# Kernel tuning notes

Measured on AMD Instinct MI355X. Metric: run time of the kernel, lower is better.

The kernel has to match this reference:

```python
import jax, jax.numpy as jnp
import numpy as np

N, F_DIM, H, K, T = 4096, 256, 256, 3, 5
START, END = 10, 3  # args.len_numerical_features, args.num_class


def setup_inputs() -> dict:
    key = jax.random.key(0)
    ks = jax.random.split(key, 8)
    s = 0.05
    x = jax.random.normal(ks[0], (N, F_DIM), dtype=jnp.float32)
    adj = jax.random.randint(ks[1], (N, N, K), 0, 2, dtype=jnp.int32)
    gnn_w = jax.random.normal(ks[2], (K, F_DIM, H), dtype=jnp.float32) * s
    gnn_b = jnp.zeros((K, H), dtype=jnp.float32)
    w_ih = jax.random.normal(ks[3], (K, 4 * H, H), dtype=jnp.float32) * s
    w_hh = jax.random.normal(ks[4], (K, 4 * H, H), dtype=jnp.float32) * s
    b_ih = jnp.zeros((K, 4 * H), dtype=jnp.float32)
    b_hh = jnp.zeros((K, 4 * H), dtype=jnp.float32)
    fc_w = jax.random.normal(ks[5], (K, F_DIM, H), dtype=jnp.float32) * s
    fc_b = jnp.zeros((K, F_DIM), dtype=jnp.float32)
    return dict(x=x, gnn_w=gnn_w, gnn_b=gnn_b, w_ih=w_ih, w_hh=w_hh,
                b_ih=b_ih, b_hh=b_hh, fc_w=fc_w, fc_b=fc_b, adj=adj)


def _gcn(x, a_bin, w, b):
    # PyG GCNConv: A_hat = A + I (self-loops added on top of existing edges,
    # weight 1), out = D^-1/2 A_hat D^-1/2 (x @ W) + b
    a = a_bin + jnp.eye(N, dtype=x.dtype)
    deg = a.sum(axis=1)
    dinv = jnp.where(deg > 0, jax.lax.rsqrt(deg), 0.0)
    a_norm = dinv[:, None] * a * dinv[None, :]
    return a_norm @ (x @ w) + b


def _lstm_last(xt, w_ih, w_hh, b_ih, b_hh):
    # batch_first LSTM over T identical inputs xt [N,H]; returns h at last step
    def step(carry, _):
        h, c = carry
        g = xt @ w_ih.T + b_ih + h @ w_hh.T + b_hh
        i, f, gg, o = jnp.split(g, 4, axis=-1)  # torch gate order: i, f, g, o
        c = jax.nn.sigmoid(f) * c + jax.nn.sigmoid(i) * jnp.tanh(gg)
        h = jax.nn.sigmoid(o) * jnp.tanh(c)
        return (h, c), None
    zero = jnp.zeros((xt.shape[0], H), dtype=xt.dtype)
    (h, c), _ = jax.lax.scan(step, (zero, zero), None, length=T)
    return h


def _sig_slice(z):
    return z.at[:, START:F_DIM - END].set(jax.nn.sigmoid(z[:, START:F_DIM - END]))


def reference(x, gnn_w, gnn_b, w_ih, w_hh, b_ih, b_hh, fc_w, fc_b, adj):
    deltas, zbars = [], []
    for k in range(K):
        a_bin = (adj[:, :, k] != 0).astype(x.dtype)
        # GCN output is identical across timesteps -> compute once
        gnn_out = _gcn(x, a_bin, gnn_w[k], gnn_b[k])
        h_last = _lstm_last(gnn_out, w_ih[k], w_hh[k], b_ih[k], b_hh[k])
        delta = jnp.tanh(h_last @ fc_w[k].T + fc_b[k])  # [N, F]
        deltas.append(delta)
        zbars.append(_sig_slice(x + delta))
    delta_z = jnp.stack(deltas, -1).mean(-1)
    res_z_bar = jnp.stack(zbars, -1)  # [N, F, K]
    pred_matrix = _sig_slice(x + delta_z)
    return pred_matrix, res_z_bar, adj
```

## Files before the change

### kernel.cpp

```cpp
#include <hip/hip_runtime.h>
#include <stdint.h>

#define NN_ 4096
#define FD 256
#define HD 256
#define KC 3
#define GD 1024
#define SA 40

typedef __attribute__((ext_vector_type(4))) unsigned int vu4;
typedef __attribute__((ext_vector_type(4))) int vi4;
typedef __attribute__((ext_vector_type(4))) float vf4;
typedef __attribute__((ext_vector_type(4))) unsigned short vus4;
typedef __attribute__((ext_vector_type(8))) short short8;
typedef __attribute__((ext_vector_type(4))) float f32x4;

typedef __attribute__((address_space(1))) const void GV;
typedef __attribute__((address_space(3))) void LV;
__device__ __forceinline__ void gl16(const void* g, void* l) {
    __builtin_amdgcn_global_load_lds((GV*)g, (LV*)l, 16, 0, 0);
}

__device__ __forceinline__ float b2f(unsigned short u) {
    unsigned int v = ((unsigned int)u) << 16; float f; __builtin_memcpy(&f, &v, 4); return f;
}
__device__ __forceinline__ unsigned short f2b(float x) {
    unsigned int u; __builtin_memcpy(&u, &x, 4);
    u = (u + 0x7FFFu + ((u >> 16) & 1u)) >> 16;
    return (unsigned short)u;
}
__device__ __forceinline__ void cvt8(const float* __restrict__ g, unsigned short* o) {
    vf4 a = *(const vf4*)g, b = *(const vf4*)(g + 4);
    o[0] = f2b(a[0]); o[1] = f2b(a[1]); o[2] = f2b(a[2]); o[3] = f2b(a[3]);
    o[4] = f2b(b[0]); o[5] = f2b(b[1]); o[6] = f2b(b[2]); o[7] = f2b(b[3]);
}
__device__ __forceinline__ float sigm(float v) { return 1.f / (1.f + __expf(-v)); }

__global__ __launch_bounds__(256) void adj_pass(const int* __restrict__ adj,
        float* __restrict__ adj_out, unsigned short* __restrict__ abk,
        float* __restrict__ dinv) {
    const int i = blockIdx.x, t = threadIdx.x;
    const int* src = adj + (size_t)i * 12288;
    float* dstf = adj_out + (size_t)i * 12288;
    float s0 = 0.f, s1 = 0.f, s2 = 0.f;
#pragma unroll
    for (int it = 0; it < 4; ++it) {
        int jq = (it * 256 + t) * 4;
        vi4 a = *(const vi4*)(src + jq * 3);
        vi4 b = *(const vi4*)(src + jq * 3 + 4);
        vi4 c = *(const vi4*)(src + jq * 3 + 8);
        int vv[12] = {a[0],a[1],a[2],a[3],b[0],b[1],b[2],b[3],c[0],c[1],c[2],c[3]};
        float ff[12];
#pragma unroll
        for (int e = 0; e < 12; ++e) ff[e] = vv[e] ? 1.f : 0.f;
        vf4 w0 = {ff[0],ff[1],ff[2],ff[3]}, w1 = {ff[4],ff[5],ff[6],ff[7]}, w2 = {ff[8],ff[9],ff[10],ff[11]};
        *(vf4*)(dstf + jq * 3) = w0; *(vf4*)(dstf + jq * 3 + 4) = w1; *(vf4*)(dstf + jq * 3 + 8) = w2;
#pragma unroll
        for (int k = 0; k < 3; ++k) {
            vus4 w;
            w[0] = vv[k]     ? (unsigned short)0x3F80 : (unsigned short)0;
            w[1] = vv[3 + k] ? (unsigned short)0x3F80 : (unsigned short)0;
            w[2] = vv[6 + k] ? (unsigned short)0x3F80 : (unsigned short)0;
            w[3] = vv[9 + k] ? (unsigned short)0x3F80 : (unsigned short)0;
            *(vus4*)(abk + ((size_t)(k * NN_ + i)) * NN_ + jq) = w;
        }
        s0 += ff[0] + ff[3] + ff[6] + ff[9];
        s1 += ff[1] + ff[4] + ff[7] + ff[10];
        s2 += ff[2] + ff[5] + ff[8] + ff[11];
    }
    __shared__ float r0[256], r1[256], r2[256];
    r0[t] = s0; r1[t] = s1; r2[t] = s2;
    __syncthreads();
    for (int off = 128; off > 0; off >>= 1) {
        if (t < off) { r0[t] += r0[t + off]; r1[t] += r1[t + off]; r2[t] += r2[t + off]; }
        __syncthreads();
    }
    if (t == 0) {
        dinv[i]            = 1.f / sqrtf(1.f + r0[0]);
        dinv[NN_ + i]      = 1.f / sqrtf(1.f + r1[0]);
        dinv[2 * NN_ + i]  = 1.f / sqrtf(1.f + r2[0]);
    }
}

__global__ __launch_bounds__(256) void wcvt(const float* __restrict__ wih,
        const float* __restrict__ whh, const float* __restrict__ fcw,
        unsigned short* __restrict__ wb) {
    size_t e = ((size_t)blockIdx.x * 256 + threadIdx.x) * 8;
    const float* src; size_t off;
    if (e < 786432)       { src = wih; off = e; }
    else if (e < 1572864) { src = whh; off = e - 786432; }
    else                  { src = fcw; off = e - 1572864; }
    alignas(16) unsigned short o[8];
    cvt8(src + off, o);
    *(vu4*)(wb + e) = *(vu4*)o;
}

__global__ __launch_bounds__(256) void gemm_xw(const float* __restrict__ x,
        const float* __restrict__ gw, const float* __restrict__ dinv,
        unsigned short* __restrict__ yT) {
    __shared__ __align__(16) unsigned short sA[64 * SA], sB[64 * SA];
    const int bi = blockIdx.x, bj = blockIdx.y, k = blockIdx.z;
    const int t = threadIdx.x, lane = t & 63, wave = t >> 6;
    const int m = lane & 15, q = lane >> 4, ko = q * 8;
    const int h0 = bj * 64;
    f32x4 acc[4] = {};
    const float* A0 = x + (size_t)(bi * 64) * FD;
    const float* B0 = gw + (size_t)k * FD * HD;
    const int r = t >> 2, c8 = (t & 3) << 3;
    const int fB = t >> 3, c8B = (t & 7) << 3;
    for (int k0 = 0; k0 < FD; k0 += 32) {
        alignas(16) unsigned short tA[8], tB[8];
        cvt8(A0 + (size_t)r * FD + k0 + c8, tA);
        *(vu4*)(sA + r * SA + c8) = *(vu4*)tA;
        cvt8(B0 + (size_t)(k0 + fB) * HD + h0 + c8B, tB);
#pragma unroll
        for (int e = 0; e < 8; ++e) sB[(c8B + e) * SA + fB] = tB[e];
        __syncthreads();
        short8 af = *(const short8*)(sA + (wave * 16 + m) * SA + ko);
#pragma unroll
        for (int ct = 0; ct < 4; ++ct) {
            short8 bf = *(const short8*)(sB + (ct * 16 + m) * SA + ko);
            acc[ct] = __builtin_amdgcn_mfma_f32_16x16x32_bf16(af, bf, acc[ct], 0, 0, 0);
        }
        __syncthreads();
    }
    unsigned short* yTk = yT + (size_t)k * HD * NN_;
#pragma unroll
    for (int ct = 0; ct < 4; ++ct)
#pragma unroll
        for (int r2 = 0; r2 < 4; ++r2) {
            int col = h0 + ct * 16 + m;
            int row = bi * 64 + wave * 16 + q * 4 + r2;
            yTk[(size_t)col * NN_ + row] = f2b(acc[ct][r2] * dinv[(size_t)k * NN_ + row]);
        }
}

__global__ __launch_bounds__(256) void gemm_agg(const unsigned short* __restrict__ abk,
        const unsigned short* __restrict__ yT, unsigned short* __restrict__ pbuf) {
    __shared__ __align__(16) unsigned short sA[128 * 32], sB[128 * 32];
    const int d = blockIdx.x;
    const int w = (d & 7) * 96 + (d >> 3);
    const int bh = w & 1, bi = (w >> 1) & 31, z = w >> 6;
    const int k = z >> 2, s = z & 3;
    const int t = threadIdx.x, lane = t & 63, wave = t >> 6;
    const int wi = wave & 1, wh = wave >> 1;
    const int m = lane & 15, q = lane >> 4, ko = q * 8;
    const int i0 = bi * 128, h0 = bh * 128, jbase = s * 1024;
    f32x4 acc[4][4] = {};
    const int lrow = lane >> 2, lcol = (lane & 3) << 3;
    const unsigned short* Ag0 = abk + ((size_t)(k * NN_ + i0 + wave * 32 + lrow)) * NN_ + jbase + lcol;
    const unsigned short* Ag1 = Ag0 + (size_t)16 * NN_;
    const unsigned short* Bg0 = yT + ((size_t)(k * 256 + h0 + wave * 32 + lrow)) * NN_ + jbase + lcol;
    const unsigned short* Bg1 = Bg0 + (size_t)16 * NN_;
    unsigned short* lA0 = sA + (wave * 32) * 32;
    unsigned short* lA1 = lA0 + 16 * 32;
    unsigned short* lB0 = sB + (wave * 32) * 32;
    unsigned short* lB1 = lB0 + 16 * 32;
    for (int j0 = 0; j0 < 1024; j0 += 32) {
        gl16(Ag0 + j0, lA0);
        gl16(Ag1 + j0, lA1);
        gl16(Bg0 + j0, lB0);
        gl16(Bg1 + j0, lB1);
        __syncthreads();
        short8 af[4], bf[4];
#pragma unroll
        for (int rt = 0; rt < 4; ++rt)
            af[rt] = *(const short8*)(sA + (wi * 64 + rt * 16 + m) * 32 + ko);
#pragma unroll
        for (int ct = 0; ct < 4; ++ct)
            bf[ct] = *(const short8*)(sB + (wh * 64 + ct * 16 + m) * 32 + ko);
#pragma unroll
        for (int ct = 0; ct < 4; ++ct)
#pragma unroll
            for (int rt = 0; rt < 4; ++rt)
                acc[rt][ct] = __builtin_amdgcn_mfma_f32_16x16x32_bf16(af[rt], bf[ct], acc[rt][ct], 0, 0, 0);
        __syncthreads();
    }
    const int addself = ((bi >> 3) == s);
#pragma unroll
    for (int rt = 0; rt < 4; ++rt)
#pragma unroll
        for (int ct = 0; ct < 4; ++ct)
#pragma unroll
            for (int r2 = 0; r2 < 4; ++r2) {
                int row = i0 + wi * 64 + rt * 16 + q * 4 + r2;
                int col = h0 + wh * 64 + ct * 16 + m;
                float v = acc[rt][ct][r2];
                if (addself) v += b2f(yT[((size_t)k * 256 + col) * NN_ + row]);
                pbuf[(((size_t)s * 3 + k) * NN_ + row) * 256 + col] = f2b(v);
            }
}

__global__ __launch_bounds__(256) void agg_reduce(const unsigned short* __restrict__ pbuf,
        const float* __restrict__ dinv, const float* __restrict__ gnnb,
        unsigned short* __restrict__ xt) {
    size_t e8 = ((size_t)blockIdx.x * 256 + threadIdx.x) * 8;
    int k = (int)(e8 >> 20);
    int i = (int)((e8 >> 8) & 4095);
    int h = (int)(e8 & 255);
    float di = dinv[k * NN_ + i];
    const size_t KIH = (size_t)KC * NN_ * HD;
    alignas(16) unsigned short p0[8], p1[8], p2[8], p3[8], o[8];
    *(vu4*)p0 = *(const vu4*)(pbuf + 0 * KIH + e8);
    *(vu4*)p1 = *(const vu4*)(pbuf + 1 * KIH + e8);
    *(vu4*)p2 = *(const vu4*)(pbuf + 2 * KIH + e8);
    *(vu4*)p3 = *(const vu4*)(pbuf + 3 * KIH + e8);
#pragma unroll
    for (int e = 0; e < 8; ++e) {
        float v = b2f(p0[e]) + b2f(p1[e]) + b2f(p2[e]) + b2f(p3[e]);
        o[e] = f2b(di * v + gnnb[k * HD + h + e]);
    }
    *(vu4*)(xt + e8) = *(vu4*)o;
}

__global__ __launch_bounds__(256) void lstm_mm(const unsigned short* __restrict__ A,
        const unsigned short* __restrict__ W, const float* __restrict__ b1,
        const float* __restrict__ b2, unsigned short* __restrict__ gX2,
        float* __restrict__ cbuf, unsigned short* __restrict__ hbuf, int mode) {
    __shared__ __align__(16) unsigned short sA[128 * 32];
    __shared__ __align__(16) unsigned short sB[128 * 32];
    const int d = blockIdx.x;
    const int w = (d & 7) * 96 + (d >> 3);
    const int chb = w & 7, bn = w >> 3;
    const int t = threadIdx.x, lane = t & 63, wave = t >> 6;
    const int m = lane & 15, q = lane >> 4, ko = q * 8;
    const int kk = bn >> 5;
    f32x4 acc[2][2][4] = {};
    const int lrow = lane >> 2, lcol = (lane & 3) << 3;
    const unsigned short* A0 = A + (size_t)bn * 128 * 256;
    const unsigned short* W0 = W + (size_t)kk * GD * 256 + (size_t)chb * 32 * 256;
    const unsigned short* Ag0 = A0 + (size_t)(wave * 32 + lrow) * 256 + lcol;
    const unsigned short* Ag1 = Ag0 + 16 * 256;
    const unsigned short* Bg0 = W0 + (size_t)(wave * 256 + lrow) * 256 + lcol;
    const unsigned short* Bg1 = Bg0 + 16 * 256;
    unsigned short* lA0 = sA + (wave * 32) * 32;
    unsigned short* lA1 = lA0 + 16 * 32;
    unsigned short* lB0 = sB + (wave * 32) * 32;
    unsigned short* lB1 = lB0 + 16 * 32;
    for (int k0 = 0; k0 < 256; k0 += 32) {
        gl16(Ag0 + k0, lA0);
        gl16(Ag1 + k0, lA1);
        gl16(Bg0 + k0, lB0);
        gl16(Bg1 + k0, lB1);
        __syncthreads();
        short8 af[2];
#pragma unroll
        for (int rt = 0; rt < 2; ++rt)
            af[rt] = *(const short8*)(sA + (wave * 32 + rt * 16 + m) * 32 + ko);
#pragma unroll
        for (int g = 0; g < 4; ++g)
#pragma unroll
            for (int cc = 0; cc < 2; ++cc) {
                short8 bf = *(const short8*)(sB + (g * 32 + cc * 16 + m) * 32 + ko);
#pragma unroll
                for (int rt = 0; rt < 2; ++rt)
                    acc[rt][cc][g] = __builtin_amdgcn_mfma_f32_16x16x32_bf16(af[rt], bf, acc[rt][cc][g], 0, 0, 0);
            }
        __syncthreads();
    }
#pragma unroll
    for (int rt = 0; rt < 2; ++rt)
#pragma unroll
        for (int cc = 0; cc < 2; ++cc)
#pragma unroll
            for (int r2 = 0; r2 < 4; ++r2) {
                int row = bn * 128 + wave * 32 + rt * 16 + q * 4 + r2;
                int ch = chb * 32 + cc * 16 + m;
                size_t goff = ((size_t)row * 256 + ch) * 4;
                if (mode == 0) {
                    vus4 o;
#pragma unroll
                    for (int g = 0; g < 4; ++g) {
                        float v = acc[rt][cc][g][r2]
                                + b1[kk * GD + g * 256 + ch] + b2[kk * GD + g * 256 + ch];
                        o[g] = f2b(v);
                    }
                    *(vus4*)(gX2 + goff) = o;
                } else {
                    vus4 gv = *(const vus4*)(gX2 + goff);
                    float iv = acc[rt][cc][0][r2] + b2f(gv[0]);
                    float fv = acc[rt][cc][1][r2] + b2f(gv[1]);
                    float gg = acc[rt][cc][2][r2] + b2f(gv[2]);
                    float ov = acc[rt][cc][3][r2] + b2f(gv[3]);
                    size_t coff = (size_t)row * 256 + ch;
                    float cn = sigm(fv) * cbuf[coff] + sigm(iv) * tanhf(gg);
                    cbuf[coff] = cn;
                    hbuf[coff] = f2b(sigm(ov) * tanhf(cn));
                }
            }
}

__global__ __launch_bounds__(256) void lstm_cell0(const unsigned short* __restrict__ gX2,
        float* __restrict__ cbuf, unsigned short* __restrict__ hbuf) {
    size_t e8 = ((size_t)blockIdx.x * 256 + threadIdx.x) * 8;
    size_t gb = e8 * 4;
    alignas(16) unsigned short gx[32], h8[8];
    alignas(16) float cv[8];
#pragma unroll
    for (int v = 0; v < 4; ++v)
        *(vu4*)(gx + v * 8) = *(const vu4*)(gX2 + gb + v * 8);
#pragma unroll
    for (int e = 0; e < 8; ++e) {
        float iv = b2f(gx[e * 4 + 0]), gg = b2f(gx[e * 4 + 2]), ov = b2f(gx[e * 4 + 3]);
        float cn = sigm(iv) * tanhf(gg);
        cv[e] = cn;
        h8[e] = f2b(sigm(ov) * tanhf(cn));
    }
    *(vf4*)(cbuf + e8)     = *(vf4*)cv;
    *(vf4*)(cbuf + e8 + 4) = *(vf4*)(cv + 4);
    *(vu4*)(hbuf + e8) = *(vu4*)h8;
}

__global__ __launch_bounds__(256) void gemm_nt_ep(const unsigned short* __restrict__ A,
        const unsigned short* __restrict__ W, const float* __restrict__ b1,
        unsigned short* __restrict__ outp, int COLS, int do_tanh) {
    __shared__ __align__(16) unsigned short sA[64 * 32], sB[64 * 32];
    const int bg = blockIdx.x, bn = blockIdx.y, k = blockIdx.z;
    const int t = threadIdx.x, lane = t & 63, wave = t >> 6;
    const int m = lane & 15, q = lane >> 4, ko = q * 8;
    f32x4 acc[4] = {};
    const int lrow = lane >> 2, lcol = (lane & 3) << 3;
    const unsigned short* A0 = A + ((size_t)k * NN_ + bn * 64) * HD;
    const unsigned short* W0 = W + ((size_t)k * COLS + bg * 64) * HD;
    const unsigned short* Ag = A0 + (size_t)(wave * 16 + lrow) * HD + lcol;
    const unsigned short* Bg = W0 + (size_t)(wave * 16 + lrow) * HD + lcol;
    unsigned short* lA = sA + (wave * 16) * 32;
    unsigned short* lB = sB + (wave * 16) * 32;
    for (int k0 = 0; k0 < HD; k0 += 32) {
        gl16(Ag + k0, lA);
        gl16(Bg + k0, lB);
        __syncthreads();
        short8 af = *(const short8*)(sA + (wave * 16 + m) * 32 + ko);
#pragma unroll
        for (int ct = 0; ct < 4; ++ct) {
            short8 bf = *(const short8*)(sB + (ct * 16 + m) * 32 + ko);
            acc[ct] = __builtin_amdgcn_mfma_f32_16x16x32_bf16(af, bf, acc[ct], 0, 0, 0);
        }
        __syncthreads();
    }
#pragma unroll
    for (int ct = 0; ct < 4; ++ct)
#pragma unroll
        for (int r2 = 0; r2 < 4; ++r2) {
            int col = bg * 64 + ct * 16 + m;
            int row = bn * 64 + wave * 16 + q * 4 + r2;
            float v = acc[ct][r2];
            if (b1) v += b1[(size_t)k * COLS + col];
            if (do_tanh) v = tanhf(v);
            outp[((size_t)k * NN_ + row) * COLS + col] = f2b(v);
        }
}

__global__ __launch_bounds__(256) void final_ep(const float* __restrict__ x,
        const unsigned short* __restrict__ delta, float* __restrict__ pred,
        float* __restrict__ res) {
    int idx = blockIdx.x * 256 + threadIdx.x;
    size_t base = (size_t)idx * 8;
    int f0 = (int)(base & 255);
    alignas(16) unsigned short d0[8], d1[8], d2[8];
    alignas(16) float pr[8], rs[24];
    vf4 xa = *(const vf4*)(x + base), xb = *(const vf4*)(x + base + 4);
    float xs[8] = { xa[0], xa[1], xa[2], xa[3], xb[0], xb[1], xb[2], xb[3] };
    *(vu4*)d0 = *(const vu4*)(delta + base);
    *(vu4*)d1 = *(const vu4*)(delta + (size_t)NN_ * FD + base);
    *(vu4*)d2 = *(const vu4*)(delta + 2 * (size_t)NN_ * FD + base);
#pragma unroll
    for (int e = 0; e < 8; ++e) {
        int f = f0 + e;
        bool sg = (f >= 10) && (f < 253);
        float xf = xs[e];
        float da = b2f(d0[e]), db = b2f(d1[e]), dc = b2f(d2[e]);
        float dm = (da + db + dc) * (1.f / 3.f);
        float p = xf + dm; if (sg) p = sigm(p);
        pr[e] = p;
        float z0 = xf + da; if (sg) z0 = sigm(z0);
        float z1 = xf + db; if (sg) z1 = sigm(z1);
        float z2 = xf + dc; if (sg) z2 = sigm(z2);
        rs[e * 3 + 0] = z0; rs[e * 3 + 1] = z1; rs[e * 3 + 2] = z2;
    }
    *(vf4*)(pred + base)     = *(vf4*)pr;
    *(vf4*)(pred + base + 4) = *(vf4*)(pr + 4);
    size_t rb = base * 3;
#pragma unroll
    for (int v = 0; v < 6; ++v)
        *(vf4*)(res + rb + v * 4) = *(vf4*)(rs + v * 4);
}

extern "C" void kernel_launch(void* const* d_in, const int* in_sizes, int n_in,
                              void* d_out, int out_size, void* d_ws, size_t ws_size,
                              hipStream_t stream) {
    const float* x    = (const float*)d_in[0];
    const float* gnnw = (const float*)d_in[1];
    const float* gnnb = (const float*)d_in[2];
    const float* wih  = (const float*)d_in[3];
    const float* whh  = (const float*)d_in[4];
    const float* bih  = (const float*)d_in[5];
    const float* bhh  = (const float*)d_in[6];
    const float* fcw  = (const float*)d_in[7];
    const float* fcb  = (const float*)d_in[8];
    const int*   adj  = (const int*)d_in[9];

    float* out = (float*)d_out;
    float* out_pred = out;
    float* out_res  = out + (size_t)NN_ * FD;
    float* out_adj  = out + (size_t)NN_ * FD * 4;

    char* ws = (char*)d_ws;
    float*          dinv  = (float*)ws;
    unsigned short* R1    = (unsigned short*)(ws + 49152);
    unsigned short* R2    = (unsigned short*)(ws + 6340608);
    unsigned short* wb    = (unsigned short*)(ws + 12632064);
    unsigned short* pbuf  = (unsigned short*)(ws + 16171008);
    unsigned short* gX2   = pbuf;
    unsigned short* abk   = (unsigned short*)(ws + 41336832);
    float*          cbuf  = (float*)(ws + 142000128);
    const unsigned short* wihb = wb;
    const unsigned short* whhb = wb + 786432;
    const unsigned short* fcwb = wb + 1572864;
    (void)ws_size; (void)in_sizes; (void)n_in; (void)out_size;

    wcvt<<<dim3(864), 256, 0, stream>>>(wih, whh, fcw, wb);
    adj_pass<<<dim3(4096), 256, 0, stream>>>(adj, out_adj, abk, dinv);
    gemm_xw<<<dim3(64, 4, 3), 256, 0, stream>>>(x, gnnw, dinv, R1 );
    gemm_agg<<<dim3(768), 256, 0, stream>>>(abk, R1 , pbuf);
    agg_reduce<<<dim3(1536), 256, 0, stream>>>(pbuf, dinv, gnnb, R2 );
    lstm_mm<<<dim3(768), 256, 0, stream>>>(R2 , wihb, bih, bhh, gX2, nullptr, nullptr, 0);
    lstm_cell0<<<dim3(1536), 256, 0, stream>>>(gX2, cbuf, R1 );
    for (int tstep = 1; tstep < 5; ++tstep)
        lstm_mm<<<dim3(768), 256, 0, stream>>>(R1 , whhb, nullptr, nullptr, gX2, cbuf, R1 , 1);
    gemm_nt_ep<<<dim3(4, 64, 3), 256, 0, stream>>>(R1 , fcwb, fcb, R2 , FD, 1);
    final_ep<<<dim3(512), 256, 0, stream>>>(x, R2 , out_pred, out_res);
}
```

Measured before the change: 622.3 us.

## Bit-pack adjacency for aggregation GEMM and fuse small kernels

Adjacency masks are stored as packed bits instead of a bf16 matrix, and the aggregation GEMM expands the bits into bf16 MFMA fragments from LDS. This removes a large write and re-read of the dense bf16 adjacency. Weight conversion is merged into adj_pass, the first LSTM cell update is fused into the first gate GEMM epilogue, and the FC GEMM is fused with the final sigmoid epilogue. In exchange, the inner loop does more bit-expansion ALU work, and the fused final kernel uses fewer blocks with uncoalesced stores.

```diff
diff --git a/kernel.cpp b/kernel.cpp
--- a/kernel.cpp
+++ b/kernel.cpp
@@ -7,6 +7,7 @@
 #define KC 3
 #define GD 1024
 #define SA 40
+#define BPITCH 144
 
 typedef __attribute__((ext_vector_type(4))) unsigned int vu4;
 typedef __attribute__((ext_vector_type(4))) int vi4;
@@ -37,15 +38,30 @@
 __device__ __forceinline__ float sigm(float v) { return 1.f / (1.f + __expf(-v)); }
 
 __global__ __launch_bounds__(256) void adj_pass(const int* __restrict__ adj,
-        float* __restrict__ adj_out, unsigned short* __restrict__ abk,
-        float* __restrict__ dinv) {
+        float* __restrict__ adj_out, unsigned char* __restrict__ abits,
+        float* __restrict__ dinv,
+        const float* __restrict__ wih, const float* __restrict__ whh,
+        const float* __restrict__ fcw, unsigned short* __restrict__ wb) {
     const int i = blockIdx.x, t = threadIdx.x;
+    if (i < 864) {
+        size_t e = ((size_t)i * 256 + t) * 8;
+        const float* src; size_t off;
+        if (e < 786432)       { src = wih; off = e; }
+        else if (e < 1572864) { src = whh; off = e - 786432; }
+        else                  { src = fcw; off = e - 1572864; }
+        alignas(16) unsigned short o[8];
+        cvt8(src + off, o);
+        *(vu4*)(wb + e) = *(vu4*)o;
+    }
+    __shared__ unsigned char nib[3][1024];
+    __shared__ float r0[256], r1[256], r2[256];
     const int* src = adj + (size_t)i * 12288;
     float* dstf = adj_out + (size_t)i * 12288;
     float s0 = 0.f, s1 = 0.f, s2 = 0.f;
 #pragma unroll
     for (int it = 0; it < 4; ++it) {
-        int jq = (it * 256 + t) * 4;
+        int p = it * 256 + t;
+        int jq = p * 4;
         vi4 a = *(const vi4*)(src + jq * 3);
         vi4 b = *(const vi4*)(src + jq * 3 + 4);
         vi4 c = *(const vi4*)(src + jq * 3 + 8);
@@ -57,20 +73,23 @@
         *(vf4*)(dstf + jq * 3) = w0; *(vf4*)(dstf + jq * 3 + 4) = w1; *(vf4*)(dstf + jq * 3 + 8) = w2;
 #pragma unroll
         for (int k = 0; k < 3; ++k) {
-            vus4 w;
-            w[0] = vv[k]     ? (unsigned short)0x3F80 : (unsigned short)0;
-            w[1] = vv[3 + k] ? (unsigned short)0x3F80 : (unsigned short)0;
-            w[2] = vv[6 + k] ? (unsigned short)0x3F80 : (unsigned short)0;
-            w[3] = vv[9 + k] ? (unsigned short)0x3F80 : (unsigned short)0;
-            *(vus4*)(abk + ((size_t)(k * NN_ + i)) * NN_ + jq) = w;
+            unsigned int nb = (vv[k] ? 1u : 0u) | (vv[3 + k] ? 2u : 0u)
+                            | (vv[6 + k] ? 4u : 0u) | (vv[9 + k] ? 8u : 0u);
+            nib[k][p] = (unsigned char)nb;
         }
         s0 += ff[0] + ff[3] + ff[6] + ff[9];
         s1 += ff[1] + ff[4] + ff[7] + ff[10];
         s2 += ff[2] + ff[5] + ff[8] + ff[11];
     }
-    __shared__ float r0[256], r1[256], r2[256];
     r0[t] = s0; r1[t] = s1; r2[t] = s2;
     __syncthreads();
+#pragma unroll
+    for (int k = 0; k < 3; ++k) {
+        unsigned int b0 = (unsigned int)nib[k][t * 4 + 0] | ((unsigned int)nib[k][t * 4 + 1] << 4);
+        unsigned int b1 = (unsigned int)nib[k][t * 4 + 2] | ((unsigned int)nib[k][t * 4 + 3] << 4);
+        *(unsigned short*)(abits + ((size_t)k * NN_ + i) * 512 + t * 2) =
+            (unsigned short)(b0 | (b1 << 8));
+    }
     for (int off = 128; off > 0; off >>= 1) {
         if (t < off) { r0[t] += r0[t + off]; r1[t] += r1[t + off]; r2[t] += r2[t + off]; }
         __syncthreads();
@@ -80,19 +99,6 @@
         dinv[NN_ + i]      = 1.f / sqrtf(1.f + r1[0]);
         dinv[2 * NN_ + i]  = 1.f / sqrtf(1.f + r2[0]);
     }
-}
-
-__global__ __launch_bounds__(256) void wcvt(const float* __restrict__ wih,
-        const float* __restrict__ whh, const float* __restrict__ fcw,
-        unsigned short* __restrict__ wb) {
-    size_t e = ((size_t)blockIdx.x * 256 + threadIdx.x) * 8;
-    const float* src; size_t off;
-    if (e < 786432)       { src = wih; off = e; }
-    else if (e < 1572864) { src = whh; off = e - 786432; }
-    else                  { src = fcw; off = e - 1572864; }
-    alignas(16) unsigned short o[8];
-    cvt8(src + off, o);
-    *(vu4*)(wb + e) = *(vu4*)o;
 }
 
 __global__ __launch_bounds__(256) void gemm_xw(const float* __restrict__ x,
@@ -135,9 +141,10 @@
         }
 }
 
-__global__ __launch_bounds__(256) void gemm_agg(const unsigned short* __restrict__ abk,
+__global__ __launch_bounds__(256) void gemm_agg(const unsigned char* __restrict__ abits,
         const unsigned short* __restrict__ yT, unsigned short* __restrict__ pbuf) {
-    __shared__ __align__(16) unsigned short sA[128 * 32], sB[128 * 32];
+    __shared__ __align__(16) unsigned char bitsA[128 * BPITCH];
+    __shared__ __align__(16) unsigned short sB[128 * 32];
     const int d = blockIdx.x;
     const int w = (d & 7) * 96 + (d >> 3);
     const int bh = w & 1, bi = (w >> 1) & 31, z = w >> 6;
@@ -146,26 +153,39 @@
     const int wi = wave & 1, wh = wave >> 1;
     const int m = lane & 15, q = lane >> 4, ko = q * 8;
     const int i0 = bi * 128, h0 = bh * 128, jbase = s * 1024;
+    {
+        const int row = t >> 1, half = t & 1;
+        const unsigned char* bsrc = abits + ((size_t)k * NN_ + i0 + row) * 512 + s * 128 + half * 64;
+        unsigned char* bdst = bitsA + row * BPITCH + half * 64;
+        vu4 v0 = *(const vu4*)(bsrc);
+        vu4 v1 = *(const vu4*)(bsrc + 16);
+        vu4 v2 = *(const vu4*)(bsrc + 32);
+        vu4 v3 = *(const vu4*)(bsrc + 48);
+        *(vu4*)(bdst)      = v0;
+        *(vu4*)(bdst + 16) = v1;
+        *(vu4*)(bdst + 32) = v2;
+        *(vu4*)(bdst + 48) = v3;
+    }
     f32x4 acc[4][4] = {};
     const int lrow = lane >> 2, lcol = (lane & 3) << 3;
-    const unsigned short* Ag0 = abk + ((size_t)(k * NN_ + i0 + wave * 32 + lrow)) * NN_ + jbase + lcol;
-    const unsigned short* Ag1 = Ag0 + (size_t)16 * NN_;
     const unsigned short* Bg0 = yT + ((size_t)(k * 256 + h0 + wave * 32 + lrow)) * NN_ + jbase + lcol;
     const unsigned short* Bg1 = Bg0 + (size_t)16 * NN_;
-    unsigned short* lA0 = sA + (wave * 32) * 32;
-    unsigned short* lA1 = lA0 + 16 * 32;
     unsigned short* lB0 = sB + (wave * 32) * 32;
     unsigned short* lB1 = lB0 + 16 * 32;
+    const int arow = (wi * 64 + m) * BPITCH + q;
     for (int j0 = 0; j0 < 1024; j0 += 32) {
-        gl16(Ag0 + j0, lA0);
-        gl16(Ag1 + j0, lA1);
         gl16(Bg0 + j0, lB0);
         gl16(Bg1 + j0, lB1);
         __syncthreads();
+        const int jby = j0 >> 3;
         short8 af[4], bf[4];
 #pragma unroll
-        for (int rt = 0; rt < 4; ++rt)
-            af[rt] = *(const short8*)(sA + (wi * 64 + rt * 16 + m) * 32 + ko);
+        for (int rt = 0; rt < 4; ++rt) {
+            unsigned int by = bitsA[arow + rt * 16 * BPITCH + jby];
+#pragma unroll
+            for (int e = 0; e < 8; ++e)
+                af[rt][e] = (short)(((by >> e) & 1u) ? (short)0x3F80 : (short)0);
+        }
 #pragma unroll
         for (int ct = 0; ct < 4; ++ct)
             bf[ct] = *(const short8*)(sB + (wh * 64 + ct * 16 + m) * 32 + ko);
@@ -267,22 +287,26 @@
                 int row = bn * 128 + wave * 32 + rt * 16 + q * 4 + r2;
                 int ch = chb * 32 + cc * 16 + m;
                 size_t goff = ((size_t)row * 256 + ch) * 4;
+                size_t coff = (size_t)row * 256 + ch;
                 if (mode == 0) {
+                    float v[4];
                     vus4 o;
 #pragma unroll
                     for (int g = 0; g < 4; ++g) {
-                        float v = acc[rt][cc][g][r2]
-                                + b1[kk * GD + g * 256 + ch] + b2[kk * GD + g * 256 + ch];
-                        o[g] = f2b(v);
+                        v[g] = acc[rt][cc][g][r2]
+                             + b1[kk * GD + g * 256 + ch] + b2[kk * GD + g * 256 + ch];
+                        o[g] = f2b(v[g]);
                     }
                     *(vus4*)(gX2 + goff) = o;
+                    float cn = sigm(v[0]) * tanhf(v[2]);
+                    cbuf[coff] = cn;
+                    hbuf[coff] = f2b(sigm(v[3]) * tanhf(cn));
                 } else {
                     vus4 gv = *(const vus4*)(gX2 + goff);
                     float iv = acc[rt][cc][0][r2] + b2f(gv[0]);
                     float fv = acc[rt][cc][1][r2] + b2f(gv[1]);
                     float gg = acc[rt][cc][2][r2] + b2f(gv[2]);
                     float ov = acc[rt][cc][3][r2] + b2f(gv[3]);
-                    size_t coff = (size_t)row * 256 + ch;
                     float cn = sigm(fv) * cbuf[coff] + sigm(iv) * tanhf(gg);
                     cbuf[coff] = cn;
                     hbuf[coff] = f2b(sigm(ov) * tanhf(cn));
@@ -290,51 +314,36 @@
             }
 }
 
-__global__ __launch_bounds__(256) void lstm_cell0(const unsigned short* __restrict__ gX2,
-        float* __restrict__ cbuf, unsigned short* __restrict__ hbuf) {
-    size_t e8 = ((size_t)blockIdx.x * 256 + threadIdx.x) * 8;
-    size_t gb = e8 * 4;
-    alignas(16) unsigned short gx[32], h8[8];
-    alignas(16) float cv[8];
-#pragma unroll
-    for (int v = 0; v < 4; ++v)
-        *(vu4*)(gx + v * 8) = *(const vu4*)(gX2 + gb + v * 8);
-#pragma unroll
-    for (int e = 0; e < 8; ++e) {
-        float iv = b2f(gx[e * 4 + 0]), gg = b2f(gx[e * 4 + 2]), ov = b2f(gx[e * 4 + 3]);
-        float cn = sigm(iv) * tanhf(gg);
-        cv[e] = cn;
-        h8[e] = f2b(sigm(ov) * tanhf(cn));
-    }
-    *(vf4*)(cbuf + e8)     = *(vf4*)cv;
-    *(vf4*)(cbuf + e8 + 4) = *(vf4*)(cv + 4);
-    *(vu4*)(hbuf + e8) = *(vu4*)h8;
-}
-
-__global__ __launch_bounds__(256) void gemm_nt_ep(const unsigned short* __restrict__ A,
-        const unsigned short* __restrict__ W, const float* __restrict__ b1,
-        unsigned short* __restrict__ outp, int COLS, int do_tanh) {
-    __shared__ __align__(16) unsigned short sA[64 * 32], sB[64 * 32];
-    const int bg = blockIdx.x, bn = blockIdx.y, k = blockIdx.z;
+__global__ __launch_bounds__(256) void fc_final(const unsigned short* __restrict__ A,
+        const unsigned short* __restrict__ W, const float* __restrict__ fcb,
+        const float* __restrict__ x, float* __restrict__ pred, float* __restrict__ res) {
+    __shared__ __align__(16) unsigned short sA[3][64 * 32], sB[3][64 * 32];
+    const int bg = blockIdx.x, bn = blockIdx.y;
     const int t = threadIdx.x, lane = t & 63, wave = t >> 6;
     const int m = lane & 15, q = lane >> 4, ko = q * 8;
-    f32x4 acc[4] = {};
+    f32x4 acc[3][4] = {};
     const int lrow = lane >> 2, lcol = (lane & 3) << 3;
-    const unsigned short* A0 = A + ((size_t)k * NN_ + bn * 64) * HD;
-    const unsigned short* W0 = W + ((size_t)k * COLS + bg * 64) * HD;
-    const unsigned short* Ag = A0 + (size_t)(wave * 16 + lrow) * HD + lcol;
-    const unsigned short* Bg = W0 + (size_t)(wave * 16 + lrow) * HD + lcol;
-    unsigned short* lA = sA + (wave * 16) * 32;
-    unsigned short* lB = sB + (wave * 16) * 32;
+    const unsigned short* Ag[3]; const unsigned short* Bg[3];
+#pragma unroll
+    for (int k = 0; k < 3; ++k) {
+        Ag[k] = A + ((size_t)k * NN_ + bn * 64 + wave * 16 + lrow) * HD + lcol;
+        Bg[k] = W + ((size_t)k * FD + bg * 64 + wave * 16 + lrow) * HD + lcol;
+    }
     for (int k0 = 0; k0 < HD; k0 += 32) {
-        gl16(Ag + k0, lA);
-        gl16(Bg + k0, lB);
-        __syncthreads();
-        short8 af = *(const short8*)(sA + (wave * 16 + m) * 32 + ko);
-#pragma unroll
-        for (int ct = 0; ct < 4; ++ct) {
-            short8 bf = *(const short8*)(sB + (ct * 16 + m) * 32 + ko);
-            acc[ct] = __builtin_amdgcn_mfma_f32_16x16x32_bf16(af, bf, acc[ct], 0, 0, 0);
+#pragma unroll
+        for (int k = 0; k < 3; ++k) {
+            gl16(Ag[k] + k0, sA[k] + (wave * 16) * 32);
+            gl16(Bg[k] + k0, sB[k] + (wave * 16) * 32);
+        }
+        __syncthreads();
+#pragma unroll
+        for (int k = 0; k < 3; ++k) {
+            short8 af = *(const short8*)(sA[k] + (wave * 16 + m) * 32 + ko);
+#pragma unroll
+            for (int ct = 0; ct < 4; ++ct) {
+                short8 bf = *(const short8*)(sB[k] + (ct * 16 + m) * 32 + ko);
+                acc[k][ct] = __builtin_amdgcn_mfma_f32_16x16x32_bf16(af, bf, acc[k][ct], 0, 0, 0);
+            }
         }
         __syncthreads();
     }
@@ -344,46 +353,20 @@
         for (int r2 = 0; r2 < 4; ++r2) {
             int col = bg * 64 + ct * 16 + m;
             int row = bn * 64 + wave * 16 + q * 4 + r2;
-            float v = acc[ct][r2];
-            if (b1) v += b1[(size_t)k * COLS + col];
-            if (do_tanh) v = tanhf(v);
-            outp[((size_t)k * NN_ + row) * COLS + col] = f2b(v);
-        }
-}
-
-__global__ __launch_bounds__(256) void final_ep(const float* __restrict__ x,
-        const unsigned short* __restrict__ delta, float* __restrict__ pred,
-        float* __restrict__ res) {
-    int idx = blockIdx.x * 256 + threadIdx.x;
-    size_t base = (size_t)idx * 8;
-    int f0 = (int)(base & 255);
-    alignas(16) unsigned short d0[8], d1[8], d2[8];
-    alignas(16) float pr[8], rs[24];
-    vf4 xa = *(const vf4*)(x + base), xb = *(const vf4*)(x + base + 4);
-    float xs[8] = { xa[0], xa[1], xa[2], xa[3], xb[0], xb[1], xb[2], xb[3] };
-    *(vu4*)d0 = *(const vu4*)(delta + base);
-    *(vu4*)d1 = *(const vu4*)(delta + (size_t)NN_ * FD + base);
-    *(vu4*)d2 = *(const vu4*)(delta + 2 * (size_t)NN_ * FD + base);
-#pragma unroll
-    for (int e = 0; e < 8; ++e) {
-        int f = f0 + e;
-        bool sg = (f >= 10) && (f < 253);
-        float xf = xs[e];
-        float da = b2f(d0[e]), db = b2f(d1[e]), dc = b2f(d2[e]);
-        float dm = (da + db + dc) * (1.f / 3.f);
-        float p = xf + dm; if (sg) p = sigm(p);
-        pr[e] = p;
-        float z0 = xf + da; if (sg) z0 = sigm(z0);
-        float z1 = xf + db; if (sg) z1 = sigm(z1);
-        float z2 = xf + dc; if (sg) z2 = sigm(z2);
-        rs[e * 3 + 0] = z0; rs[e * 3 + 1] = z1; rs[e * 3 + 2] = z2;
-    }
-    *(vf4*)(pred + base)     = *(vf4*)pr;
-    *(vf4*)(pred + base + 4) = *(vf4*)(pr + 4);
-    size_t rb = base * 3;
-#pragma unroll
-    for (int v = 0; v < 6; ++v)
-        *(vf4*)(res + rb + v * 4) = *(vf4*)(rs + v * 4);
+            float d0 = tanhf(acc[0][ct][r2] + fcb[col]);
+            float d1 = tanhf(acc[1][ct][r2] + fcb[FD + col]);
+            float d2 = tanhf(acc[2][ct][r2] + fcb[2 * FD + col]);
+            float xf = x[(size_t)row * FD + col];
+            bool sg = (col >= 10) && (col < 253);
+            float dm = (d0 + d1 + d2) * (1.f / 3.f);
+            float p = xf + dm; if (sg) p = sigm(p);
+            pred[(size_t)row * FD + col] = p;
+            float z0 = xf + d0; if (sg) z0 = sigm(z0);
+            float z1 = xf + d1; if (sg) z1 = sigm(z1);
+            float z2 = xf + d2; if (sg) z2 = sigm(z2);
+            size_t rb = ((size_t)row * FD + col) * 3;
+            res[rb] = z0; res[rb + 1] = z1; res[rb + 2] = z2;
+        }
 }
 
 extern "C" void kernel_launch(void* const* d_in, const int* in_sizes, int n_in,
@@ -412,22 +395,19 @@
     unsigned short* wb    = (unsigned short*)(ws + 12632064);
     unsigned short* pbuf  = (unsigned short*)(ws + 16171008);
     unsigned short* gX2   = pbuf;
-    unsigned short* abk   = (unsigned short*)(ws + 41336832);
-    float*          cbuf  = (float*)(ws + 142000128);
+    unsigned char*  abits = (unsigned char*)(ws + 41336832);
+    float*          cbuf  = (float*)(ws + 47628288);
     const unsigned short* wihb = wb;
     const unsigned short* whhb = wb + 786432;
     const unsigned short* fcwb = wb + 1572864;
     (void)ws_size; (void)in_sizes; (void)n_in; (void)out_size;
 
-    wcvt<<<dim3(864), 256, 0, stream>>>(wih, whh, fcw, wb);
-    adj_pass<<<dim3(4096), 256, 0, stream>>>(adj, out_adj, abk, dinv);
+    adj_pass<<<dim3(4096), 256, 0, stream>>>(adj, out_adj, abits, dinv, wih, whh, fcw, wb);
     gemm_xw<<<dim3(64, 4, 3), 256, 0, stream>>>(x, gnnw, dinv, R1 );
-    gemm_agg<<<dim3(768), 256, 0, stream>>>(abk, R1 , pbuf);
+    gemm_agg<<<dim3(768), 256, 0, stream>>>(abits, R1 , pbuf);
     agg_reduce<<<dim3(1536), 256, 0, stream>>>(pbuf, dinv, gnnb, R2 );
-    lstm_mm<<<dim3(768), 256, 0, stream>>>(R2 , wihb, bih, bhh, gX2, nullptr, nullptr, 0);
-    lstm_cell0<<<dim3(1536), 256, 0, stream>>>(gX2, cbuf, R1 );
+    lstm_mm<<<dim3(768), 256, 0, stream>>>(R2 , wihb, bih, bhh, gX2, cbuf, R1 , 0);
     for (int tstep = 1; tstep < 5; ++tstep)
         lstm_mm<<<dim3(768), 256, 0, stream>>>(R1 , whhb, nullptr, nullptr, gX2, cbuf, R1 , 1);
-    gemm_nt_ep<<<dim3(4, 64, 3), 256, 0, stream>>>(R1 , fcwb, fcb, R2 , FD, 1);
-    final_ep<<<dim3(512), 256, 0, stream>>>(x, R2 , out_pred, out_res);
-}
+    fc_final<<<dim3(4, 64), 256, 0, stream>>>(R1 , fcwb, fcb, x, out_pred, out_res);
+}
```

Measured after the change: 586.8 us. -5.7%, faster.
